# Performance work log

Measured on AMD Instinct MI355X. Metric: run time of the kernel, lower is better.

## Reference

```python
import jax, jax.numpy as jnp
import numpy as np

N_NODES = 50000
N_EDGES = 600000
D_FEAT = 128


def setup_inputs() -> dict:
    key = jax.random.key(0)
    k_h, k_src, k_dst, k_dt, k_norm = jax.random.split(key, 5)
    h = jax.random.normal(k_h, (N_NODES, D_FEAT), dtype=jnp.float32)
    src = jax.random.randint(k_src, (N_EDGES,), 0, N_NODES, dtype=jnp.int32)
    dst = jax.random.randint(k_dst, (N_EDGES,), 0, N_NODES, dtype=jnp.int32)
    # dt: non-negative time deltas (scaled up a bit so the decay matters)
    dt = jax.random.uniform(k_dt, (N_EDGES,), dtype=jnp.float32) * 10.0
    # norm: symmetric-normalization-like positive edge weights
    norm = jax.random.uniform(k_norm, (N_EDGES,), dtype=jnp.float32)
    decay_lam = jnp.full((1,), 0.1, dtype=jnp.float32)  # nn.Parameter(0.1)
    return {"h": h, "src": src, "dst": dst, "dt": dt, "norm": norm, "decay_lam": decay_lam}


def reference(h, src, dst, dt, norm, decay_lam):
    # lam = relu(decay_lam) + 1e-4  (scalar)
    lam = jax.nn.relu(decay_lam[0]) + 1e-4
    # per-edge temporal weight: norm * exp(-lam * dt)   [E]
    w = norm * jnp.exp(-lam * dt)
    # u_mul_e: gather source features, scale by edge weight  [E, D]
    m = h[src] * w[:, None]
    # sum-reduce messages at destination nodes  [N, D]
    h_new = jax.ops.segment_sum(m, dst, num_segments=h.shape[0])
    return h_new
```

## Files before the change

### kernel.cpp

```cpp
#include <hip/hip_runtime.h>
#include <hip/hip_bf16.h>

#define D_FEAT 128
#define BIN_SHIFT 7
#define NODES_PER_BIN 128
#define BCAP 4096
#define EPB 4096
#define T1 512
#define OVF_CAP 4096

typedef float f2v __attribute__((ext_vector_type(2)));

__device__ __forceinline__ unsigned bf16_rne(float f) {
    unsigned u = __float_as_uint(f);
    return (u + 0x7fffu + ((u >> 16) & 1u)) >> 16;
}

__global__ void conv_kernel(const float* __restrict__ h, unsigned* __restrict__ hb, int HN4) {
    int i = blockIdx.x * 256 + threadIdx.x;
    if (i >= HN4) return;
    float4 v = ((const float4*)h)[i];
    ((uint2*)hb)[i] = make_uint2(bf16_rne(v.x) | (bf16_rne(v.y) << 16),
                                 bf16_rne(v.z) | (bf16_rne(v.w) << 16));
}

__global__ void __launch_bounds__(T1)
bin_kernel(const int* __restrict__ src, const int* __restrict__ dst,
           const float* __restrict__ dt, const float* __restrict__ norm,
           const float* __restrict__ decay_lam,
           int* __restrict__ bin_cursor, unsigned long long* __restrict__ binned,
           int* __restrict__ ovf_cnt, int* __restrict__ ovf_d,
           int* __restrict__ ovf_s, float* __restrict__ ovf_w,
           int E, int NB) {
    __shared__ unsigned hist[T1];
    __shared__ unsigned tmp[T1];
    __shared__ unsigned cur[T1];
    __shared__ unsigned gbase[T1];
    __shared__ unsigned long long stage[EPB];
    __shared__ unsigned gaddr[EPB];

    int t = threadIdx.x;
    int e0 = blockIdx.x * EPB;
    int cnt_blk = min(EPB, E - e0);

    hist[t] = 0; cur[t] = 0; gbase[t] = 0;
    __syncthreads();

    float lam = fmaxf(decay_lam[0], 0.0f) + 1e-4f;

    unsigned long long ent[EPB / T1];
    int bn[EPB / T1];
    #pragma unroll
    for (int k = 0; k < EPB / T1; ++k) {
        int e = e0 + k * T1 + t;
        bn[k] = -1;
        if (e < E) {
            int s = src[e], d = dst[e];
            float w = norm[e] * expf(-lam * dt[e]);
            int b = d >> BIN_SHIFT;
            int l = d & (NODES_PER_BIN - 1);
            ent[k] = ((unsigned long long)l << 32) | (((unsigned)s << 16) | bf16_rne(w));
            bn[k] = b;
            atomicAdd(&hist[b], 1u);
        }
    }
    __syncthreads();
    tmp[t] = hist[t];
    __syncthreads();
    for (int off = 1; off < T1; off <<= 1) {
        unsigned v = (t >= off) ? tmp[t - off] : 0;
        __syncthreads();
        tmp[t] += v;
        __syncthreads();
    }
    unsigned base_t = tmp[t] - hist[t];
    if (t < NB && hist[t] > 0)
        gbase[t] = (unsigned)atomicAdd(&bin_cursor[t], (int)hist[t]);
    __syncthreads();
    tmp[t] = base_t;
    __syncthreads();

    #pragma unroll
    for (int k = 0; k < EPB / T1; ++k) {
        if (bn[k] >= 0) {
            int b = bn[k];
            unsigned loc = atomicAdd(&cur[b], 1u);
            unsigned p = tmp[b] + loc;
            unsigned gp = gbase[b] + loc;
            stage[p] = ent[k];
            if (gp < BCAP) {
                gaddr[p] = (unsigned)b * BCAP + gp;
            } else {
                gaddr[p] = 0xFFFFFFFFu;
                int o = atomicAdd(ovf_cnt, 1);
                if (o < OVF_CAP) {
                    int l = (int)(ent[k] >> 32);
                    ovf_d[o] = (b << BIN_SHIFT) | l;
                    ovf_s[o] = (int)((ent[k] >> 16) & 0xFFFFu);
                    ovf_w[o] = __uint_as_float(((unsigned)ent[k] & 0xFFFFu) << 16);
                }
            }
        }
    }
    __syncthreads();
    #pragma unroll
    for (int k = 0; k < EPB / T1; ++k) {
        int idx = k * T1 + t;
        if (idx < cnt_blk) {
            unsigned g = gaddr[idx];
            if (g != 0xFFFFFFFFu) binned[g] = stage[idx];
        }
    }
}

__global__ void __launch_bounds__(256)
sort_kernel(const unsigned long long* __restrict__ binned, const int* __restrict__ bin_cursor,
            unsigned* __restrict__ csr, int* __restrict__ offs, int* __restrict__ deg,
            int N, int NB) {
    __shared__ unsigned hist[NODES_PER_BIN];
    __shared__ unsigned tmp[NODES_PER_BIN];
    __shared__ unsigned cur[NODES_PER_BIN];
    int b = blockIdx.x;
    int t = threadIdx.x;
    int cnt = min(bin_cursor[b], BCAP);
    if (t < NODES_PER_BIN) { hist[t] = 0; cur[t] = 0; }
    __syncthreads();
    size_t base_in = (size_t)b * BCAP;
    for (int i = t; i < cnt; i += 256) {
        int l = (int)(binned[base_in + i] >> 32);
        atomicAdd(&hist[l], 1u);
    }
    __syncthreads();
    if (t < NODES_PER_BIN) tmp[t] = hist[t];
    __syncthreads();
    for (int off = 1; off < NODES_PER_BIN; off <<= 1) {
        unsigned v = 0;
        if (t < NODES_PER_BIN && t >= off) v = tmp[t - off];
        __syncthreads();
        if (t < NODES_PER_BIN) tmp[t] += v;
        __syncthreads();
    }
    if (t < NODES_PER_BIN) {
        int node = (b << BIN_SHIFT) + t;
        unsigned loff = tmp[t] - hist[t];
        if (node < N) {
            offs[node] = b * BCAP + (int)loff;
            deg[node]  = (int)hist[t];
        }
        tmp[t] = loff;
    }
    __syncthreads();
    for (int i = t; i < cnt; i += 256) {
        unsigned long long e = binned[base_in + i];
        int l = (int)(e >> 32);
        unsigned p = tmp[l] + atomicAdd(&cur[l], 1u);
        csr[base_in + p] = (unsigned)e;
    }
}

__global__ void __launch_bounds__(256)
gather_kernel2(const unsigned* __restrict__ hb, const int* __restrict__ offs,
               const int* __restrict__ deg, const unsigned* __restrict__ csr,
               const int* __restrict__ bin_cursor,
               const int* __restrict__ ovf_cnt, const int* __restrict__ ovf_d,
               const int* __restrict__ ovf_s, const float* __restrict__ ovf_w,
               float* __restrict__ out, int N) {
    int node = blockIdx.x * 4 + (threadIdx.x >> 6);
    if (node >= N) return;
    int lane = threadIdx.x & 63;
    int dg = deg[node];
    int base = offs[node];
    int m = min(dg, 64);

    unsigned pu = 0;
    if (lane < m) pu = csr[base + lane];
    int mr = (m + 7) & ~7;

    float accx = 0.0f, accy = 0.0f;
    for (int j = 0; j < mr; j += 8) {
        unsigned u0 = __shfl(pu, j + 0, 64);
        unsigned u1 = __shfl(pu, j + 1, 64);
        unsigned u2 = __shfl(pu, j + 2, 64);
        unsigned u3 = __shfl(pu, j + 3, 64);
        unsigned u4 = __shfl(pu, j + 4, 64);
        unsigned u5 = __shfl(pu, j + 5, 64);
        unsigned u6 = __shfl(pu, j + 6, 64);
        unsigned u7 = __shfl(pu, j + 7, 64);
        unsigned v0 = hb[(size_t)(u0 >> 16) * 64 + lane];
        unsigned v1 = hb[(size_t)(u1 >> 16) * 64 + lane];
        unsigned v2 = hb[(size_t)(u2 >> 16) * 64 + lane];
        unsigned v3 = hb[(size_t)(u3 >> 16) * 64 + lane];
        unsigned v4 = hb[(size_t)(u4 >> 16) * 64 + lane];
        unsigned v5 = hb[(size_t)(u5 >> 16) * 64 + lane];
        unsigned v6 = hb[(size_t)(u6 >> 16) * 64 + lane];
        unsigned v7 = hb[(size_t)(u7 >> 16) * 64 + lane];
        #define ACC(u, v)                                             \
        {   float wf = __uint_as_float((u) << 16);                    \
            float vx = __uint_as_float((v) << 16);                    \
            float vy = __uint_as_float((v) & 0xffff0000u);            \
            accx += vx * wf; accy += vy * wf; }
        ACC(u0, v0) ACC(u1, v1) ACC(u2, v2) ACC(u3, v3)
        ACC(u4, v4) ACC(u5, v5) ACC(u6, v6) ACC(u7, v7)
        #undef ACC
    }
    for (int j = 64; j < dg; ++j) {
        unsigned u = csr[base + j];
        float wf = __uint_as_float(u << 16);
        unsigned v = hb[(size_t)(u >> 16) * 64 + lane];
        accx += __uint_as_float(v << 16) * wf;
        accy += __uint_as_float(v & 0xffff0000u) * wf;
    }
    if (bin_cursor[node >> BIN_SHIFT] > BCAP) {
        int oc = min(*ovf_cnt, OVF_CAP);
        for (int o = 0; o < oc; ++o) {
            if (ovf_d[o] == node) {
                float we = ovf_w[o];
                unsigned v = hb[(size_t)ovf_s[o] * 64 + lane];
                accx += __uint_as_float(v << 16) * we;
                accy += __uint_as_float(v & 0xffff0000u) * we;
            }
        }
    }
    f2v r;
    r.x = accx; r.y = accy;
    __builtin_nontemporal_store(r, (f2v*)(out + (size_t)node * D_FEAT) + lane);
}


__global__ void degree_kernel(const int* __restrict__ dst, int* __restrict__ deg, int E) {
    int e = blockIdx.x * blockDim.x + threadIdx.x;
    if (e >= E) return;
    atomicAdd(&deg[dst[e]], 1);
}

__global__ void scan_blocks(const int* __restrict__ deg, int* __restrict__ offs,
                            int* __restrict__ blockSums, int N) {
    __shared__ int tmp[256];
    int tid = threadIdx.x;
    int gid = blockIdx.x * 256 + tid;
    int v = (gid < N) ? deg[gid] : 0;
    tmp[tid] = v;
    __syncthreads();
    for (int off = 1; off < 256; off <<= 1) {
        int t = (tid >= off) ? tmp[tid - off] : 0;
        __syncthreads();
        tmp[tid] += t;
        __syncthreads();
    }
    if (gid < N) offs[gid] = tmp[tid] - v;
    if (tid == 255) blockSums[blockIdx.x] = tmp[255];
}

__global__ void scan_sums(int* __restrict__ blockSums, int* __restrict__ blockOffs, int nb) {
    __shared__ int tmp[256];
    int tid = threadIdx.x;
    int v = (tid < nb) ? blockSums[tid] : 0;
    tmp[tid] = v;
    __syncthreads();
    for (int off = 1; off < 256; off <<= 1) {
        int t = (tid >= off) ? tmp[tid - off] : 0;
        __syncthreads();
        tmp[tid] += t;
        __syncthreads();
    }
    if (tid < nb) blockOffs[tid] = tmp[tid] - v;
}

__global__ void scan_fixup(int* __restrict__ offs, const int* __restrict__ blockOffs,
                           int* __restrict__ cursor, int N) {
    int gid = blockIdx.x * 256 + threadIdx.x;
    if (gid >= N) return;
    int o = offs[gid] + blockOffs[blockIdx.x];
    offs[gid] = o;
    cursor[gid] = o;
}

__global__ void bucket_kernel(const int* __restrict__ src, const int* __restrict__ dst,
                              const float* __restrict__ dt, const float* __restrict__ norm,
                              const float* __restrict__ decay_lam,
                              int* __restrict__ cursor, float2* __restrict__ pairs, int E) {
    int e = blockIdx.x * blockDim.x + threadIdx.x;
    if (e >= E) return;
    float lam = fmaxf(decay_lam[0], 0.0f) + 1e-4f;
    float w = norm[e] * expf(-lam * dt[e]);
    int d = dst[e];
    int pos = atomicAdd(&cursor[d], 1);
    float2 p;
    p.x = __int_as_float(src[e]);
    p.y = w;
    pairs[pos] = p;
}

__global__ void __launch_bounds__(256)
gather_kernel(const float* __restrict__ h,
              const int* __restrict__ offs, const int* __restrict__ deg,
              const float2* __restrict__ pairs, float* __restrict__ out, int N) {
    int node = blockIdx.x * 4 + (threadIdx.x >> 6);
    if (node >= N) return;
    int lane = threadIdx.x & 63;
    int start = offs[node];
    int end = start + deg[node];
    float accx = 0.0f, accy = 0.0f;
    for (int j = start; j < end; ++j) {
        float2 p = pairs[j];
        int s = __float_as_int(p.x);
        float we = p.y;
        float2 v = ((const float2*)(h + (size_t)s * D_FEAT))[lane];
        accx += v.x * we;
        accy += v.y * we;
    }
    float2 r; r.x = accx; r.y = accy;
    ((float2*)(out + (size_t)node * D_FEAT))[lane] = r;
}

extern "C" void kernel_launch(void* const* d_in, const int* in_sizes, int n_in,
                              void* d_out, int out_size, void* d_ws, size_t ws_size,
                              hipStream_t stream) {
    const float* h         = (const float*)d_in[0];
    const int*   src       = (const int*)d_in[1];
    const int*   dst       = (const int*)d_in[2];
    const float* dt        = (const float*)d_in[3];
    const float* norm      = (const float*)d_in[4];
    const float* decay_lam = (const float*)d_in[5];
    float* out = (float*)d_out;

    const int E  = in_sizes[1];
    const int HN = in_sizes[0];
    const int N  = out_size / D_FEAT;
    const int NB = (N + NODES_PER_BIN - 1) >> BIN_SHIFT;

    auto align64 = [](size_t x) { return (x + 63) & ~(size_t)63; };
    size_t sz_binc = align64((size_t)NB * 4);
    size_t sz_ovfc = 64;
    size_t sz_ovf  = align64((size_t)OVF_CAP * 4);
    size_t sz_offs = align64((size_t)N * 4);
    size_t sz_binn = align64((size_t)NB * BCAP * 8);
    size_t sz_csr  = align64((size_t)NB * BCAP * 4);
    size_t sz_hb   = align64((size_t)HN * 2);
    size_t need = sz_binc + sz_ovfc + 3 * sz_ovf + 2 * sz_offs + sz_binn + sz_csr + sz_hb;

    if (ws_size >= need && N <= 65536 && (HN & 3) == 0) {
        char* ws = (char*)d_ws;
        int* bin_cursor = (int*)ws;                 ws += sz_binc;
        int* ovf_cnt    = (int*)ws;                 ws += sz_ovfc;
        int* ovf_d      = (int*)ws;                 ws += sz_ovf;
        int* ovf_s      = (int*)ws;                 ws += sz_ovf;
        float* ovf_w    = (float*)ws;               ws += sz_ovf;
        int* offs       = (int*)ws;                 ws += sz_offs;
        int* deg        = (int*)ws;                 ws += sz_offs;
        unsigned long long* binned = (unsigned long long*)ws;  ws += sz_binn;
        unsigned* csr   = (unsigned*)ws;            ws += sz_csr;
        unsigned* hb    = (unsigned*)ws;

        hipMemsetAsync(bin_cursor, 0, sz_binc + sz_ovfc, stream);

        conv_kernel<<<(HN / 4 + 255) / 256, 256, 0, stream>>>(h, hb, HN / 4);
        bin_kernel<<<(E + EPB - 1) / EPB, T1, 0, stream>>>(
            src, dst, dt, norm, decay_lam, bin_cursor, binned,
            ovf_cnt, ovf_d, ovf_s, ovf_w, E, NB);
        sort_kernel<<<NB, 256, 0, stream>>>(binned, bin_cursor, csr, offs, deg, N, NB);
        gather_kernel2<<<(N + 3) / 4, 256, 0, stream>>>(
            hb, offs, deg, csr, bin_cursor, ovf_cnt, ovf_d, ovf_s, ovf_w, out, N);
    } else {
        const int nb = (N + 255) / 256;
        char* ws = (char*)d_ws;
        int*    dega      = (int*)ws;     ws += (size_t)N * 4;
        int*    offsa     = (int*)ws;     ws += (size_t)N * 4;
        int*    cursor    = (int*)ws;     ws += (size_t)N * 4;
        int*    blockSums = (int*)ws;     ws += 256 * 4;
        int*    blockOffs = (int*)ws;     ws += 256 * 4;
        float2* pairs     = (float2*)ws;

        hipMemsetAsync(dega, 0, (size_t)N * 4, stream);
        degree_kernel<<<(E + 255) / 256, 256, 0, stream>>>(dst, dega, E);
        scan_blocks<<<nb, 256, 0, stream>>>(dega, offsa, blockSums, N);
        scan_sums<<<1, 256, 0, stream>>>(blockSums, blockOffs, nb);
        scan_fixup<<<nb, 256, 0, stream>>>(offsa, blockOffs, cursor, N);
        bucket_kernel<<<(E + 255) / 256, 256, 0, stream>>>(
            src, dst, dt, norm, decay_lam, cursor, pairs, E);
        gather_kernel<<<(N + 3) / 4, 256, 0, stream>>>(h, offsa, dega, pairs, out, N);
    }
}
```

Measured before the change: 130.5 us.

## Fuse bf16 conversion into binning and fuse per-bin sort with gather

Merges the feature bf16 conversion into the binning kernel as extra leading blocks. It also merges the per-bin counting sort with the gather: each bin's CSR now lives in shared memory, with per-node segments padded to multiples of 8, and 8 waves gather the bin's 128 nodes. This removes two launches and the global csr/offs/deg round trip. In exchange, only NB≈391 blocks of 512 threads run the gather, which lowers parallelism and gives coarser load balance than the old one-wave-per-node grid.

```diff
diff --git a/kernel.cpp b/kernel.cpp
--- a/kernel.cpp
+++ b/kernel.cpp
@@ -7,6 +7,7 @@
 #define BCAP 4096
 #define EPB 4096
 #define T1 512
+#define CSR_L_CAP 5120
 #define OVF_CAP 4096
 
 typedef float f2v __attribute__((ext_vector_type(2)));
@@ -16,22 +17,16 @@
     return (u + 0x7fffu + ((u >> 16) & 1u)) >> 16;
 }
 
-__global__ void conv_kernel(const float* __restrict__ h, unsigned* __restrict__ hb, int HN4) {
-    int i = blockIdx.x * 256 + threadIdx.x;
-    if (i >= HN4) return;
-    float4 v = ((const float4*)h)[i];
-    ((uint2*)hb)[i] = make_uint2(bf16_rne(v.x) | (bf16_rne(v.y) << 16),
-                                 bf16_rne(v.z) | (bf16_rne(v.w) << 16));
-}
-
 __global__ void __launch_bounds__(T1)
-bin_kernel(const int* __restrict__ src, const int* __restrict__ dst,
-           const float* __restrict__ dt, const float* __restrict__ norm,
-           const float* __restrict__ decay_lam,
-           int* __restrict__ bin_cursor, unsigned long long* __restrict__ binned,
-           int* __restrict__ ovf_cnt, int* __restrict__ ovf_d,
-           int* __restrict__ ovf_s, float* __restrict__ ovf_w,
-           int E, int NB) {
+conv_bin_kernel(const float* __restrict__ h,
+                const int* __restrict__ src, const int* __restrict__ dst,
+                const float* __restrict__ dt, const float* __restrict__ norm,
+                const float* __restrict__ decay_lam,
+                unsigned* __restrict__ hb,
+                int* __restrict__ bin_cursor, unsigned long long* __restrict__ binned,
+                int* __restrict__ ovf_cnt, int* __restrict__ ovf_d,
+                int* __restrict__ ovf_s, float* __restrict__ ovf_w,
+                int E, int HN4, int convBlocks, int NB) {
     __shared__ unsigned hist[T1];
     __shared__ unsigned tmp[T1];
     __shared__ unsigned cur[T1];
@@ -40,7 +35,17 @@
     __shared__ unsigned gaddr[EPB];
 
     int t = threadIdx.x;
-    int e0 = blockIdx.x * EPB;
+    if (blockIdx.x < convBlocks) {
+        int i = blockIdx.x * T1 + t;
+        if (i < HN4) {
+            float4 v = ((const float4*)h)[i];
+            ((uint2*)hb)[i] = make_uint2(bf16_rne(v.x) | (bf16_rne(v.y) << 16),
+                                         bf16_rne(v.z) | (bf16_rne(v.w) << 16));
+        }
+        return;
+    }
+
+    int e0 = (blockIdx.x - convBlocks) * EPB;
     int cnt_blk = min(EPB, E - e0);
 
     hist[t] = 0; cur[t] = 0; gbase[t] = 0;
@@ -113,117 +118,114 @@
     }
 }
 
-__global__ void __launch_bounds__(256)
-sort_kernel(const unsigned long long* __restrict__ binned, const int* __restrict__ bin_cursor,
-            unsigned* __restrict__ csr, int* __restrict__ offs, int* __restrict__ deg,
-            int N, int NB) {
+__global__ void __launch_bounds__(T1)
+sort_gather_kernel(const unsigned long long* __restrict__ binned,
+                   const int* __restrict__ bin_cursor,
+                   const unsigned* __restrict__ hb,
+                   const int* __restrict__ ovf_cnt, const int* __restrict__ ovf_d,
+                   const int* __restrict__ ovf_s, const float* __restrict__ ovf_w,
+                   float* __restrict__ out, int N) {
     __shared__ unsigned hist[NODES_PER_BIN];
-    __shared__ unsigned tmp[NODES_PER_BIN];
+    __shared__ unsigned padoff[NODES_PER_BIN];
     __shared__ unsigned cur[NODES_PER_BIN];
+    __shared__ unsigned csr_l[CSR_L_CAP];
+
     int b = blockIdx.x;
     int t = threadIdx.x;
     int cnt = min(bin_cursor[b], BCAP);
+
     if (t < NODES_PER_BIN) { hist[t] = 0; cur[t] = 0; }
-    __syncthreads();
+    for (int i = t; i < CSR_L_CAP; i += T1) csr_l[i] = 0;
+    __syncthreads();
+
+    unsigned long long ent[BCAP / T1];
     size_t base_in = (size_t)b * BCAP;
-    for (int i = t; i < cnt; i += 256) {
-        int l = (int)(binned[base_in + i] >> 32);
-        atomicAdd(&hist[l], 1u);
-    }
-    __syncthreads();
-    if (t < NODES_PER_BIN) tmp[t] = hist[t];
+    #pragma unroll
+    for (int k = 0; k < BCAP / T1; ++k) {
+        int idx = k * T1 + t;
+        ent[k] = ~0ull;
+        if (idx < cnt) {
+            unsigned long long e = binned[base_in + idx];
+            ent[k] = e;
+            atomicAdd(&hist[(int)(e >> 32)], 1u);
+        }
+    }
+    __syncthreads();
+
+    unsigned pc = 0;
+    if (t < NODES_PER_BIN) { pc = (hist[t] + 7u) & ~7u; padoff[t] = pc; }
     __syncthreads();
     for (int off = 1; off < NODES_PER_BIN; off <<= 1) {
         unsigned v = 0;
-        if (t < NODES_PER_BIN && t >= off) v = tmp[t - off];
-        __syncthreads();
-        if (t < NODES_PER_BIN) tmp[t] += v;
-        __syncthreads();
-    }
-    if (t < NODES_PER_BIN) {
-        int node = (b << BIN_SHIFT) + t;
-        unsigned loff = tmp[t] - hist[t];
-        if (node < N) {
-            offs[node] = b * BCAP + (int)loff;
-            deg[node]  = (int)hist[t];
-        }
-        tmp[t] = loff;
-    }
-    __syncthreads();
-    for (int i = t; i < cnt; i += 256) {
-        unsigned long long e = binned[base_in + i];
-        int l = (int)(e >> 32);
-        unsigned p = tmp[l] + atomicAdd(&cur[l], 1u);
-        csr[base_in + p] = (unsigned)e;
-    }
-}
-
-__global__ void __launch_bounds__(256)
-gather_kernel2(const unsigned* __restrict__ hb, const int* __restrict__ offs,
-               const int* __restrict__ deg, const unsigned* __restrict__ csr,
-               const int* __restrict__ bin_cursor,
-               const int* __restrict__ ovf_cnt, const int* __restrict__ ovf_d,
-               const int* __restrict__ ovf_s, const float* __restrict__ ovf_w,
-               float* __restrict__ out, int N) {
-    int node = blockIdx.x * 4 + (threadIdx.x >> 6);
-    if (node >= N) return;
-    int lane = threadIdx.x & 63;
-    int dg = deg[node];
-    int base = offs[node];
-    int m = min(dg, 64);
-
-    unsigned pu = 0;
-    if (lane < m) pu = csr[base + lane];
-    int mr = (m + 7) & ~7;
-
-    float accx = 0.0f, accy = 0.0f;
-    for (int j = 0; j < mr; j += 8) {
-        unsigned u0 = __shfl(pu, j + 0, 64);
-        unsigned u1 = __shfl(pu, j + 1, 64);
-        unsigned u2 = __shfl(pu, j + 2, 64);
-        unsigned u3 = __shfl(pu, j + 3, 64);
-        unsigned u4 = __shfl(pu, j + 4, 64);
-        unsigned u5 = __shfl(pu, j + 5, 64);
-        unsigned u6 = __shfl(pu, j + 6, 64);
-        unsigned u7 = __shfl(pu, j + 7, 64);
-        unsigned v0 = hb[(size_t)(u0 >> 16) * 64 + lane];
-        unsigned v1 = hb[(size_t)(u1 >> 16) * 64 + lane];
-        unsigned v2 = hb[(size_t)(u2 >> 16) * 64 + lane];
-        unsigned v3 = hb[(size_t)(u3 >> 16) * 64 + lane];
-        unsigned v4 = hb[(size_t)(u4 >> 16) * 64 + lane];
-        unsigned v5 = hb[(size_t)(u5 >> 16) * 64 + lane];
-        unsigned v6 = hb[(size_t)(u6 >> 16) * 64 + lane];
-        unsigned v7 = hb[(size_t)(u7 >> 16) * 64 + lane];
-        #define ACC(u, v)                                             \
-        {   float wf = __uint_as_float((u) << 16);                    \
-            float vx = __uint_as_float((v) << 16);                    \
-            float vy = __uint_as_float((v) & 0xffff0000u);            \
-            accx += vx * wf; accy += vy * wf; }
-        ACC(u0, v0) ACC(u1, v1) ACC(u2, v2) ACC(u3, v3)
-        ACC(u4, v4) ACC(u5, v5) ACC(u6, v6) ACC(u7, v7)
-        #undef ACC
-    }
-    for (int j = 64; j < dg; ++j) {
-        unsigned u = csr[base + j];
-        float wf = __uint_as_float(u << 16);
-        unsigned v = hb[(size_t)(u >> 16) * 64 + lane];
-        accx += __uint_as_float(v << 16) * wf;
-        accy += __uint_as_float(v & 0xffff0000u) * wf;
-    }
-    if (bin_cursor[node >> BIN_SHIFT] > BCAP) {
-        int oc = min(*ovf_cnt, OVF_CAP);
-        for (int o = 0; o < oc; ++o) {
-            if (ovf_d[o] == node) {
-                float we = ovf_w[o];
-                unsigned v = hb[(size_t)ovf_s[o] * 64 + lane];
-                accx += __uint_as_float(v << 16) * we;
-                accy += __uint_as_float(v & 0xffff0000u) * we;
+        if (t < NODES_PER_BIN && t >= off) v = padoff[t - off];
+        __syncthreads();
+        if (t < NODES_PER_BIN) padoff[t] += v;
+        __syncthreads();
+    }
+    if (t < NODES_PER_BIN) padoff[t] -= pc;
+    __syncthreads();
+
+    #pragma unroll
+    for (int k = 0; k < BCAP / T1; ++k) {
+        if (ent[k] != ~0ull) {
+            int l = (int)(ent[k] >> 32);
+            unsigned p = padoff[l] + atomicAdd(&cur[l], 1u);
+            csr_l[p] = (unsigned)ent[k];
+        }
+    }
+    __syncthreads();
+
+    int wid = t >> 6;
+    int lane = t & 63;
+    int nodes = min(NODES_PER_BIN, N - (b << BIN_SHIFT));
+    bool ovf_bin = bin_cursor[b] > BCAP;
+
+    for (int l = wid; l < nodes; l += 8) {
+        unsigned base = padoff[l];
+        unsigned mr = (hist[l] + 7u) & ~7u;
+        float accx = 0.0f, accy = 0.0f;
+        for (unsigned j = 0; j < mr; j += 8) {
+            unsigned u0 = csr_l[base + j + 0];
+            unsigned u1 = csr_l[base + j + 1];
+            unsigned u2 = csr_l[base + j + 2];
+            unsigned u3 = csr_l[base + j + 3];
+            unsigned u4 = csr_l[base + j + 4];
+            unsigned u5 = csr_l[base + j + 5];
+            unsigned u6 = csr_l[base + j + 6];
+            unsigned u7 = csr_l[base + j + 7];
+            unsigned v0 = hb[(size_t)(u0 >> 16) * 64 + lane];
+            unsigned v1 = hb[(size_t)(u1 >> 16) * 64 + lane];
+            unsigned v2 = hb[(size_t)(u2 >> 16) * 64 + lane];
+            unsigned v3 = hb[(size_t)(u3 >> 16) * 64 + lane];
+            unsigned v4 = hb[(size_t)(u4 >> 16) * 64 + lane];
+            unsigned v5 = hb[(size_t)(u5 >> 16) * 64 + lane];
+            unsigned v6 = hb[(size_t)(u6 >> 16) * 64 + lane];
+            unsigned v7 = hb[(size_t)(u7 >> 16) * 64 + lane];
+            #define ACC(u, v)                                             \
+            {   float wf = __uint_as_float((u) << 16);                    \
+                float vx = __uint_as_float((v) << 16);                    \
+                float vy = __uint_as_float((v) & 0xffff0000u);            \
+                accx += vx * wf; accy += vy * wf; }
+            ACC(u0, v0) ACC(u1, v1) ACC(u2, v2) ACC(u3, v3)
+            ACC(u4, v4) ACC(u5, v5) ACC(u6, v6) ACC(u7, v7)
+            #undef ACC
+        }
+        int node = (b << BIN_SHIFT) + l;
+        if (ovf_bin) {
+            int oc = min(*ovf_cnt, OVF_CAP);
+            for (int o = 0; o < oc; ++o) {
+                if (ovf_d[o] == node) {
+                    float we = ovf_w[o];
+                    unsigned v = hb[(size_t)ovf_s[o] * 64 + lane];
+                    accx += __uint_as_float(v << 16) * we;
+                    accy += __uint_as_float(v & 0xffff0000u) * we;
+                }
             }
         }
-    }
-    f2v r;
-    r.x = accx; r.y = accy;
-    __builtin_nontemporal_store(r, (f2v*)(out + (size_t)node * D_FEAT) + lane);
+        f2v r;
+        r.x = accx; r.y = accy;
+        __builtin_nontemporal_store(r, (f2v*)(out + (size_t)node * D_FEAT) + lane);
+    }
 }
 
 
@@ -333,34 +335,31 @@
     size_t sz_binc = align64((size_t)NB * 4);
     size_t sz_ovfc = 64;
     size_t sz_ovf  = align64((size_t)OVF_CAP * 4);
-    size_t sz_offs = align64((size_t)N * 4);
     size_t sz_binn = align64((size_t)NB * BCAP * 8);
-    size_t sz_csr  = align64((size_t)NB * BCAP * 4);
     size_t sz_hb   = align64((size_t)HN * 2);
-    size_t need = sz_binc + sz_ovfc + 3 * sz_ovf + 2 * sz_offs + sz_binn + sz_csr + sz_hb;
-
-    if (ws_size >= need && N <= 65536 && (HN & 3) == 0) {
+    size_t need = sz_binc + sz_ovfc + 3 * sz_ovf + sz_binn + sz_hb;
+
+    if (ws_size >= need && N <= 65536 && (HN & 3) == 0 && NB <= T1) {
         char* ws = (char*)d_ws;
         int* bin_cursor = (int*)ws;                 ws += sz_binc;
         int* ovf_cnt    = (int*)ws;                 ws += sz_ovfc;
         int* ovf_d      = (int*)ws;                 ws += sz_ovf;
         int* ovf_s      = (int*)ws;                 ws += sz_ovf;
         float* ovf_w    = (float*)ws;               ws += sz_ovf;
-        int* offs       = (int*)ws;                 ws += sz_offs;
-        int* deg        = (int*)ws;                 ws += sz_offs;
         unsigned long long* binned = (unsigned long long*)ws;  ws += sz_binn;
-        unsigned* csr   = (unsigned*)ws;            ws += sz_csr;
         unsigned* hb    = (unsigned*)ws;
 
         hipMemsetAsync(bin_cursor, 0, sz_binc + sz_ovfc, stream);
 
-        conv_kernel<<<(HN / 4 + 255) / 256, 256, 0, stream>>>(h, hb, HN / 4);
-        bin_kernel<<<(E + EPB - 1) / EPB, T1, 0, stream>>>(
-            src, dst, dt, norm, decay_lam, bin_cursor, binned,
-            ovf_cnt, ovf_d, ovf_s, ovf_w, E, NB);
-        sort_kernel<<<NB, 256, 0, stream>>>(binned, bin_cursor, csr, offs, deg, N, NB);
-        gather_kernel2<<<(N + 3) / 4, 256, 0, stream>>>(
-            hb, offs, deg, csr, bin_cursor, ovf_cnt, ovf_d, ovf_s, ovf_w, out, N);
+        const int HN4 = HN / 4;
+        const int convBlocks = (HN4 + T1 - 1) / T1;
+        const int binBlocks  = (E + EPB - 1) / EPB;
+        conv_bin_kernel<<<convBlocks + binBlocks, T1, 0, stream>>>(
+            h, src, dst, dt, norm, decay_lam, hb, bin_cursor, binned,
+            ovf_cnt, ovf_d, ovf_s, ovf_w, E, HN4, convBlocks, NB);
+
+        sort_gather_kernel<<<NB, T1, 0, stream>>>(
+            binned, bin_cursor, hb, ovf_cnt, ovf_d, ovf_s, ovf_w, out, N);
     } else {
         const int nb = (N + 255) / 256;
         char* ws = (char*)d_ws;
```

After: 128.1 us. No clear change (-1.8%).
